# Kernel optimization log

Hardware: AMD Instinct MI355X
Metric: run time of the kernel (lower is better)

Reference implementation:

```python
import jax, jax.numpy as jnp
import numpy as np

N, E, IN, ED, H, L, OUT = 50000, 600000, 16, 4, 128, 4, 3


def setup_inputs() -> dict:
    key = jax.random.key(0)
    ks = jax.random.split(key, 16)
    s = 0.05  # small init scale for numerical stability
    return {
        "x": jax.random.normal(ks[0], (N, IN), jnp.float32),
        "edge_index": jax.random.randint(ks[1], (2, E), 0, N, jnp.int64 if jax.config.jax_enable_x64 else jnp.int32),
        "edge_attr": jax.random.normal(ks[2], (E, ED), jnp.float32),
        "lin_in_w": jax.random.normal(ks[3], (IN, H), jnp.float32) * s,
        "lin_in_b": jnp.zeros((H,), jnp.float32),
        "msg_w1": jax.random.normal(ks[4], (L, H + ED, H), jnp.float32) * s,
        "msg_b1": jnp.zeros((L, H), jnp.float32),
        "msg_w2": jax.random.normal(ks[5], (L, H, H), jnp.float32) * s,
        "msg_b2": jnp.zeros((L, H), jnp.float32),
        "upd_w1": jax.random.normal(ks[6], (L, 2 * H, H), jnp.float32) * s,
        "upd_b1": jnp.zeros((L, H), jnp.float32),
        "upd_w2": jax.random.normal(ks[7], (L, H, H), jnp.float32) * s,
        "upd_b2": jnp.zeros((L, H), jnp.float32),
        "head_w1": jax.random.normal(ks[8], (H, H), jnp.float32) * s,
        "head_b1": jnp.zeros((H,), jnp.float32),
        "head_w2": jax.random.normal(ks[9], (H, OUT), jnp.float32) * s,
        "head_b2": jnp.zeros((OUT,), jnp.float32),
    }


def reference(x, edge_index, edge_attr, lin_in_w, lin_in_b,
              msg_w1, msg_b1, msg_w2, msg_b2,
              upd_w1, upd_b1, upd_w2, upd_b2,
              head_w1, head_b1, head_w2, head_b2):
    n = x.shape[0]
    src, dst = edge_index[0], edge_index[1]  # PyG: message from src (x_j), aggregate at dst
    h = jax.nn.relu(x @ lin_in_w + lin_in_b)  # [N, H]
    # mean-aggregation denominator (0-degree nodes -> divide by 1, sum is 0 anyway)
    cnt = jax.ops.segment_sum(jnp.ones((src.shape[0],), h.dtype), dst, num_segments=n)
    cnt = jnp.maximum(cnt, 1.0)[:, None]
    for l in range(msg_w1.shape[0]):
        mi = jnp.concatenate([h[src], edge_attr], axis=1)          # [E, H+ED] edge gather
        m = jax.nn.relu(mi @ msg_w1[l] + msg_b1[l])
        m = jax.nn.relu(m @ msg_w2[l] + msg_b2[l])                 # [E, H] per-edge message
        agg = jax.ops.segment_sum(m, dst, num_segments=n) / cnt    # [N, H] scatter-mean
        u = jnp.concatenate([h, agg], axis=1)
        u = jax.nn.relu(u @ upd_w1[l] + upd_b1[l])
        u = u @ upd_w2[l] + upd_b2[l]
        h = jax.nn.relu(u + h)  # residual + relu; dropout is eval-mode identity
    o = jax.nn.relu(h @ head_w1 + head_b1)
    return jax.nn.relu(o @ head_w2 + head_b2)  # [N, OUT]
```

## Files before the change

### kernel.cpp

```cpp
#include <hip/hip_runtime.h>


typedef _Float16 f16x8 __attribute__((ext_vector_type(8)));
typedef _Float16 f16x2 __attribute__((ext_vector_type(2)));
typedef __fp16  fp16x2 __attribute__((ext_vector_type(2)));
typedef float f32x4 __attribute__((ext_vector_type(4)));

__device__ inline uint pk2(float a, float b) {
  fp16x2 h = __builtin_amdgcn_cvt_pkrtz(a, b);
  return __builtin_bit_cast(uint, h);
}
__device__ inline ushort f2h(float f) {
  fp16x2 h = __builtin_amdgcn_cvt_pkrtz(f, 0.f);
  return (ushort)__builtin_bit_cast(uint, h);
}
__device__ inline f16x2 bch(uint u) { return __builtin_bit_cast(f16x2, u); }

template <int NT>
__device__ inline void stage_w(ushort* Ws, const ushort* __restrict__ Wt, int t) {
#pragma unroll
  for (int i = t; i < 2048; i += NT) {
    int r = i >> 4, c = i & 15;
    *(uint4*)&Ws[r * 136 + c * 8] = *(const uint4*)&Wt[r * 128 + c * 8];
  }
}
__device__ inline void mfma_4ks(f32x4* acc, const ushort* A, const ushort* Ws,
                                int wave, int lane) {
  int cl = lane & 15, kq = (lane >> 4) * 8;
  int arow = (wave * 16 + cl) * 136;
#pragma unroll
  for (int ks = 0; ks < 4; ++ks) {
    f16x8 af = *(const f16x8*)&A[arow + ks * 32 + kq];
#pragma unroll
    for (int ct = 0; ct < 8; ++ct) {
      f16x8 bf = *(const f16x8*)&Ws[(ct * 16 + cl) * 136 + ks * 32 + kq];
      acc[ct] = __builtin_amdgcn_mfma_f32_16x16x32_f16(af, bf, acc[ct], 0, 0, 0);
    }
  }
}
__device__ inline void mfma_regA(f32x4* acc, const f16x8* af, const ushort* Ws,
                                 int lane) {
  int cl = lane & 15, kq = (lane >> 4) * 8;
#pragma unroll
  for (int ks = 0; ks < 4; ++ks) {
#pragma unroll
    for (int ct = 0; ct < 8; ++ct) {
      f16x8 bf = *(const f16x8*)&Ws[(ct * 16 + cl) * 136 + ks * 32 + kq];
      acc[ct] = __builtin_amdgcn_mfma_f32_16x16x32_f16(af[ks], bf, acc[ct], 0, 0, 0);
    }
  }
}

__global__ __launch_bounds__(256) void count_int_kernel(const int* __restrict__ dst,
                                                        int* __restrict__ cnti, int E) {
  int e = blockIdx.x * 256 + threadIdx.x;
  if (e < E) atomicAdd(&cnti[dst[e]], 1);
}

__global__ __launch_bounds__(256) void scan_block_sum(const int* __restrict__ cnti,
                                                      int* __restrict__ bsum, int N) {
  int i = blockIdx.x * 256 + threadIdx.x;
  int v = (i < N) ? cnti[i] : 0;
#pragma unroll
  for (int o = 1; o < 64; o <<= 1) v += __shfl_xor(v, o);
  __shared__ int wsum[4];
  if ((threadIdx.x & 63) == 0) wsum[threadIdx.x >> 6] = v;
  __syncthreads();
  if (threadIdx.x == 0) bsum[blockIdx.x] = wsum[0] + wsum[1] + wsum[2] + wsum[3];
}
__global__ __launch_bounds__(256) void scan_partials(int* __restrict__ bsum, int nb) {
  __shared__ int s[256];
  int t = threadIdx.x;
  int v = (t < nb) ? bsum[t] : 0;
  s[t] = v;
  __syncthreads();
  for (int o = 1; o < 256; o <<= 1) {
    int u = (t >= o) ? s[t - o] : 0;
    __syncthreads();
    s[t] += u;
    __syncthreads();
  }
  if (t < nb) bsum[t] = s[t] - v;
}
__global__ __launch_bounds__(256) void scan_final(const int* __restrict__ cnti,
                                                  const int* __restrict__ bsum,
                                                  int* __restrict__ rowptr,
                                                  float* __restrict__ invf, int N) {
  __shared__ int s[256];
  int i = blockIdx.x * 256 + threadIdx.x;
  int t = threadIdx.x;
  int v = (i < N) ? cnti[i] : 0;
  s[t] = v;
  __syncthreads();
  for (int o = 1; o < 256; o <<= 1) {
    int u = (t >= o) ? s[t - o] : 0;
    __syncthreads();
    s[t] += u;
    __syncthreads();
  }
  if (i < N) {
    rowptr[i] = bsum[blockIdx.x] + s[t] - v;
    invf[i] = 1.f / (float)max(v, 1);
  }
}

__global__ __launch_bounds__(256) void scatter_kernel(
    const int* __restrict__ src, const int* __restrict__ dst,
    const float4* __restrict__ ea, const int* __restrict__ rowptr,
    int* __restrict__ tmpc, int* __restrict__ srcs, int* __restrict__ dsts,
    float4* __restrict__ eas, int E) {
  int e = blockIdx.x * 256 + threadIdx.x;
  if (e >= E) return;
  int d = dst[e];
  int r = atomicAdd(&tmpc[d], 1);
  int p = rowptr[d] + r;
  srcs[p] = src[e];
  dsts[p] = d;
  eas[p] = ea[e];
}

struct WPtrs { const float* src[22]; };
__global__ __launch_bounds__(256) void wconv_kernel(WPtrs p, ushort* __restrict__ wtb,
                                                    ushort* __restrict__ wlin) {
  int m = blockIdx.y;
  int idx = blockIdx.x * 256 + threadIdx.x;
  if (m == 21) {
    if (idx >= 4096) return;
    int n = idx >> 5, k = idx & 31;
    wlin[idx] = (k < 16) ? f2h(p.src[21][k * 128 + n]) : (ushort)0;
  } else {
    int n = idx >> 7, k = idx & 127;
    wtb[(size_t)m * 16384 + idx] = f2h(p.src[m][k * 128 + n]);
  }
}

__global__ __launch_bounds__(256) void lin_hw_kernel(
    const float* __restrict__ x, const ushort* __restrict__ wlin,
    const float* __restrict__ lb, const ushort* __restrict__ mw1t,
    const float* __restrict__ mb1, float* __restrict__ h,
    ushort* __restrict__ hwb, int N) {
  __shared__ char smem[69632] __attribute__((aligned(16)));
  ushort* xb  = (ushort*)smem;
  ushort* wsl = (ushort*)(smem + 4096);
  ushort* As1 = (ushort*)(smem + 12288);
  ushort* Ws  = (ushort*)(smem + 34816);
  int t = threadIdx.x, lane = t & 63, wave = t >> 6;
  int m0 = blockIdx.x * 64;
  int cl = lane & 15, kq = (lane >> 4) * 8;

  for (int i = t; i < 2048; i += 256) {
    int row = i >> 5, c = i & 31;
    int m = m0 + row;
    xb[i] = (c < 16 && m < N) ? f2h(x[(size_t)m * 16 + c]) : (ushort)0;
  }
  for (int i = t; i < 4096 / 8; i += 256)
    *(uint4*)&wsl[i * 8] = *(const uint4*)&wlin[i * 8];
  stage_w<256>(Ws, mw1t, t);
  __syncthreads();

  f32x4 acc[8];
#pragma unroll
  for (int i = 0; i < 8; ++i)
#pragma unroll
    for (int j = 0; j < 4; ++j) acc[i][j] = 0.f;
  {
    f16x8 af = *(const f16x8*)&xb[(wave * 16 + cl) * 32 + kq];
#pragma unroll
    for (int ct = 0; ct < 8; ++ct) {
      f16x8 bf = *(const f16x8*)&wsl[(ct * 16 + cl) * 32 + kq];
      acc[ct] = __builtin_amdgcn_mfma_f32_16x16x32_f16(af, bf, acc[ct], 0, 0, 0);
    }
  }
#pragma unroll
  for (int reg = 0; reg < 4; ++reg) {
    int row = wave * 16 + (lane >> 4) * 4 + reg;
    int m = m0 + row;
#pragma unroll
    for (int ct = 0; ct < 8; ++ct) {
      int col = ct * 16 + cl;
      float v = fmaxf(acc[ct][reg] + lb[col], 0.f);
      if (m < N) h[(size_t)m * 128 + col] = v;
      As1[row * 136 + col] = f2h(v);
    }
  }
  __syncthreads();
  f32x4 acc2[8];
#pragma unroll
  for (int i = 0; i < 8; ++i)
#pragma unroll
    for (int j = 0; j < 4; ++j) acc2[i][j] = 0.f;
  mfma_4ks(acc2, As1, Ws, wave, lane);
#pragma unroll
  for (int reg = 0; reg < 4; ++reg) {
    int m = m0 + wave * 16 + (lane >> 4) * 4 + reg;
    if (m >= N) continue;
#pragma unroll
    for (int ct = 0; ct < 8; ++ct) {
      int col = ct * 16 + cl;
      hwb[(size_t)m * 128 + col] = f2h(acc2[ct][reg] + mb1[col]);
    }
  }
}

__global__ __launch_bounds__(256, 4) void edge_kernel_v9(
    const ushort* __restrict__ hw, const float4* __restrict__ eas,
    const int* __restrict__ srcs, const int* __restrict__ dsts,
    const ushort* __restrict__ W2t, const float* __restrict__ Wea,
    const float* __restrict__ b2, float* __restrict__ agg, int E) {
  __shared__ ushort Ws[128 * 136];
  __shared__ uint weaH[64][4];
  __shared__ float b2s[128];
  __shared__ int dss[130];
  int t = threadIdx.x, lane = t & 63, wave = t >> 6;
  int cl = lane & 15, g = lane >> 4;
  int p0 = blockIdx.x * 128;
  int base = wave * 32;

  int e0 = p0 + base + cl, e1 = e0 + 16;
  bool v0 = e0 < E, v1 = e1 < E;
  int s0 = v0 ? srcs[e0] : 0, s1 = v1 ? srcs[e1] : 0;
  float4 ea0 = v0 ? eas[e0] : make_float4(0.f, 0.f, 0.f, 0.f);
  float4 ea1 = v1 ? eas[e1] : make_float4(0.f, 0.f, 0.f, 0.f);
  uint4 hv0[4], hv1[4];
  {
    const ushort* h0 = hw + (size_t)s0 * 128 + g * 8;
    const ushort* h1 = hw + (size_t)s1 * 128 + g * 8;
#pragma unroll
    for (int ks = 0; ks < 4; ++ks) {
      hv0[ks] = v0 ? *(const uint4*)&h0[ks * 32] : make_uint4(0, 0, 0, 0);
      hv1[ks] = v1 ? *(const uint4*)&h1[ks * 32] : make_uint4(0, 0, 0, 0);
    }
  }

  stage_w<256>(Ws, W2t, t);
  if (t < 64) {
    weaH[t][0] = pk2(Wea[2 * t], Wea[2 * t + 1]);
    weaH[t][1] = pk2(Wea[128 + 2 * t], Wea[128 + 2 * t + 1]);
    weaH[t][2] = pk2(Wea[256 + 2 * t], Wea[256 + 2 * t + 1]);
    weaH[t][3] = pk2(Wea[384 + 2 * t], Wea[384 + 2 * t + 1]);
  }
  if (t < 128) {
    b2s[t] = b2[t];
    dss[1 + t] = (p0 + t < E) ? dsts[p0 + t] : -1;
  }
  if (t == 0) dss[0] = (p0 > 0) ? dsts[p0 - 1] : -2;
  if (t == 1) dss[129] = (p0 + 128 < E) ? dsts[p0 + 128] : -3;
  __syncthreads();

  uint e0b[4] = {pk2(ea0.x, ea0.x), pk2(ea0.y, ea0.y), pk2(ea0.z, ea0.z), pk2(ea0.w, ea0.w)};
  uint e1b[4] = {pk2(ea1.x, ea1.x), pk2(ea1.y, ea1.y), pk2(ea1.z, ea1.z), pk2(ea1.w, ea1.w)};

  f16x8 af0[4], af1[4];
  f16x2 z2 = {};
#pragma unroll
  for (int ks = 0; ks < 4; ++ks) {
    union { uint u32[4]; f16x8 v; } o0, o1;
    const uint* q0 = (const uint*)&hv0[ks];
    const uint* q1 = (const uint*)&hv1[ks];
    int k2b = ks * 16 + g * 4;
#pragma unroll
    for (int p = 0; p < 4; ++p) {
      uint4 w4 = *(const uint4*)&weaH[k2b + p][0];
      f16x2 m0h = bch(q0[p]);
      f16x2 m1h = bch(q1[p]);
      m0h += bch(e0b[0]) * bch(w4.x); m1h += bch(e1b[0]) * bch(w4.x);
      m0h += bch(e0b[1]) * bch(w4.y); m1h += bch(e1b[1]) * bch(w4.y);
      m0h += bch(e0b[2]) * bch(w4.z); m1h += bch(e1b[2]) * bch(w4.z);
      m0h += bch(e0b[3]) * bch(w4.w); m1h += bch(e1b[3]) * bch(w4.w);
      o0.u32[p] = __builtin_bit_cast(uint, __builtin_elementwise_max(m0h, z2));
      o1.u32[p] = __builtin_bit_cast(uint, __builtin_elementwise_max(m1h, z2));
    }
    af0[ks] = o0.v; af1[ks] = o1.v;
  }

  f32x4 acc0[8], acc1[8];
#pragma unroll
  for (int i = 0; i < 8; ++i)
#pragma unroll
    for (int j = 0; j < 4; ++j) { acc0[i][j] = 0.f; acc1[i][j] = 0.f; }
#pragma unroll
  for (int ks = 0; ks < 4; ++ks) {
#pragma unroll
    for (int ct = 0; ct < 8; ++ct) {
      f16x8 bf = *(const f16x8*)&Ws[(ct * 16 + cl) * 136 + ks * 32 + g * 8];
      acc0[ct] = __builtin_amdgcn_mfma_f32_16x16x32_f16(af0[ks], bf, acc0[ct], 0, 0, 0);
      acc1[ct] = __builtin_amdgcn_mfma_f32_16x16x32_f16(af1[ks], bf, acc1[ct], 0, 0, 0);
    }
  }

#pragma unroll
  for (int ct = 0; ct < 8; ++ct) {
    float bb = b2s[ct * 16 + cl];
#pragma unroll
    for (int reg = 0; reg < 4; ++reg) {
      acc0[ct][reg] = fmaxf(acc0[ct][reg] + bb, 0.f);
      acc1[ct][reg] = fmaxf(acc1[ct][reg] + bb, 0.f);
    }
  }

  int rloc = lane & 31;
  int dmy = dss[1 + base + rloc];
  int dpv = dss[base + rloc];
  int dafter = dss[1 + base + 32];
  unsigned long long bm = __ballot(dmy != dpv);
  unsigned mask32 = (unsigned)bm | 1u;
  bool firstClosed = ((unsigned)bm & 1u) != 0;
  while (mask32) {
    int rOff = __ffs(mask32) - 1;
    unsigned rest = mask32 & (mask32 - 1);
    int eOff = rest ? (__ffs(rest) - 1) : 32;
    mask32 = rest;
    int d = __shfl(dmy, rOff);
    if (d < 0) continue;
    bool openL = (rOff == 0) && !firstClosed;
    bool openR = (eOff == 32) && (dafter == d);
    float ps[8];
#pragma unroll
    for (int ct = 0; ct < 8; ++ct) ps[ct] = 0.f;
#pragma unroll
    for (int reg = 0; reg < 4; ++reg) {
      int r0w = g * 4 + reg;
      bool in0 = (r0w >= rOff) && (r0w < eOff);
      bool in1 = (r0w + 16 >= rOff) && (r0w + 16 < eOff);
#pragma unroll
      for (int ct = 0; ct < 8; ++ct) {
        if (in0) ps[ct] += acc0[ct][reg];
        if (in1) ps[ct] += acc1[ct][reg];
      }
    }
#pragma unroll
    for (int ct = 0; ct < 8; ++ct) {
      ps[ct] += __shfl_xor(ps[ct], 16);
      ps[ct] += __shfl_xor(ps[ct], 32);
    }
    if (g == 0) {
      float* ag = &agg[(size_t)d * 128 + cl];
      if (openL || openR) {
#pragma unroll
        for (int ct = 0; ct < 8; ++ct) atomicAdd(&ag[ct * 16], ps[ct]);
      } else {
#pragma unroll
        for (int ct = 0; ct < 8; ++ct) ag[ct * 16] = ps[ct];
      }
    }
  }
}

__global__ __launch_bounds__(512, 2) void fused_update(
    const float* __restrict__ h, const float* __restrict__ agg,
    const float* __restrict__ inv, const ushort* __restrict__ Wu1a,
    const ushort* __restrict__ Wu1b, const ushort* __restrict__ Wu2,
    const float* __restrict__ b1, const float* __restrict__ b2,
    const ushort* __restrict__ Wn, const float* __restrict__ bn,
    float* __restrict__ h_out, ushort* __restrict__ hwb,
    const float* __restrict__ hw2, const float* __restrict__ hb2,
    float* __restrict__ out, int N, int is_last) {
  __shared__ char smem[69632] __attribute__((aligned(16)));
  ushort* As1 = (ushort*)smem;
  ushort* Ws  = (ushort*)(smem + 34816);
  float* otile = (float*)smem;
  float* w2s   = (float*)(smem + 66560);
  int t = threadIdx.x, lane = t & 63, wave = t >> 6;
  int m0 = blockIdx.x * 128;
  int cl = lane & 15, g = lane >> 4;

  int m2r = m0 + wave * 16 + cl;
  bool mv = m2r < N;
  float sI = mv ? inv[m2r] : 0.f;
  float4 ga[8];
  {
    const float* gp = agg + (size_t)(mv ? m2r : 0) * 128 + g * 8;
#pragma unroll
    for (int ks = 0; ks < 4; ++ks) {
      ga[ks * 2 + 0] = *(const float4*)&gp[ks * 32];
      ga[ks * 2 + 1] = *(const float4*)&gp[ks * 32 + 4];
    }
  }

  {
    int row = t >> 2, q = t & 3;
    int m = m0 + row;
    union { uint u32[16]; uint4 u4[4]; } a;
    if (m < N) {
      const float* hp = h + (size_t)m * 128 + q * 32;
#pragma unroll
      for (int j = 0; j < 8; ++j) {
        float4 hv = *(const float4*)&hp[j * 4];
        a.u32[j * 2 + 0] = pk2(hv.x, hv.y);
        a.u32[j * 2 + 1] = pk2(hv.z, hv.w);
      }
    } else {
#pragma unroll
      for (int j = 0; j < 16; ++j) a.u32[j] = 0;
    }
#pragma unroll
    for (int j = 0; j < 4; ++j)
      *(uint4*)&As1[row * 136 + q * 32 + j * 8] = a.u4[j];
  }
  stage_w<512>(Ws, Wu1a, t);
  __syncthreads();

  f32x4 acc[8];
#pragma unroll
  for (int i = 0; i < 8; ++i)
#pragma unroll
    for (int j = 0; j < 4; ++j) acc[i][j] = 0.f;
  mfma_4ks(acc, As1, Ws, wave, lane);
  __syncthreads();
  stage_w<512>(Ws, Wu1b, t);
  f16x8 af2[4];
#pragma unroll
  for (int ks = 0; ks < 4; ++ks) {
    union { uint u32[4]; f16x8 v; } o;
    const float* f = (const float*)&ga[ks * 2];
#pragma unroll
    for (int j = 0; j < 4; ++j)
      o.u32[j] = pk2(f[j * 2] * sI, f[j * 2 + 1] * sI);
    af2[ks] = o.v;
  }
  __syncthreads();
  mfma_regA(acc, af2, Ws, lane);
  __syncthreads();

#pragma unroll
  for (int reg = 0; reg < 4; ++reg) {
    int row = wave * 16 + g * 4 + reg;
#pragma unroll
    for (int ct = 0; ct < 8; ++ct) {
      int col = ct * 16 + cl;
      As1[row * 136 + col] = f2h(fmaxf(acc[ct][reg] + b1[col], 0.f));
    }
  }
  stage_w<512>(Ws, Wu2, t);
  __syncthreads();

  f32x4 acc2[8];
#pragma unroll
  for (int i = 0; i < 8; ++i)
#pragma unroll
    for (int j = 0; j < 4; ++j) acc2[i][j] = 0.f;
  mfma_4ks(acc2, As1, Ws, wave, lane);
  __syncthreads();

#pragma unroll
  for (int reg = 0; reg < 4; ++reg) {
    int row = wave * 16 + g * 4 + reg;
    int m = m0 + row;
#pragma unroll
    for (int ct = 0; ct < 8; ++ct) {
      int col = ct * 16 + cl;
      float v = acc2[ct][reg] + b2[col];
      if (m < N) v += h[(size_t)m * 128 + col];
      v = fmaxf(v, 0.f);
      if (!is_last && m < N) h_out[(size_t)m * 128 + col] = v;
      As1[row * 136 + col] = f2h(v);
    }
  }
  stage_w<512>(Ws, Wn, t);
  __syncthreads();

  f32x4 acc3[8];
#pragma unroll
  for (int i = 0; i < 8; ++i)
#pragma unroll
    for (int j = 0; j < 4; ++j) acc3[i][j] = 0.f;
  mfma_4ks(acc3, As1, Ws, wave, lane);

  if (!is_last) {
#pragma unroll
    for (int reg = 0; reg < 4; ++reg) {
      int m = m0 + wave * 16 + g * 4 + reg;
      if (m >= N) continue;
#pragma unroll
      for (int ct = 0; ct < 8; ++ct) {
        int col = ct * 16 + cl;
        hwb[(size_t)m * 128 + col] = f2h(acc3[ct][reg] + bn[col]);
      }
    }
  } else {
    __syncthreads();
#pragma unroll
    for (int reg = 0; reg < 4; ++reg) {
      int row = wave * 16 + g * 4 + reg;
#pragma unroll
      for (int ct = 0; ct < 8; ++ct) {
        int col = ct * 16 + cl;
        otile[row * 130 + col] = fmaxf(acc3[ct][reg] + bn[col], 0.f);
      }
    }
    for (int i = t; i < 384; i += 512) w2s[i] = hw2[i];
    __syncthreads();
    if (t < 384) {
      int row = t / 3, c = t % 3;
      int m = m0 + row;
      if (m < N) {
        float s = hb2[c];
#pragma unroll 16
        for (int k = 0; k < 128; ++k) s += otile[row * 130 + k] * w2s[k * 3 + c];
        out[(size_t)m * 3 + c] = fmaxf(s, 0.f);
      }
    }
  }
}

extern "C" void kernel_launch(void* const* d_in, const int* in_sizes, int n_in,
                              void* d_out, int out_size, void* d_ws, size_t ws_size,
                              hipStream_t stream) {
  const float* x       = (const float*)d_in[0];
  const int*   ei      = (const int*)  d_in[1];
  const float* ea      = (const float*)d_in[2];
  const float* lin_w   = (const float*)d_in[3];
  const float* lin_b   = (const float*)d_in[4];
  const float* msg_w1  = (const float*)d_in[5];
  const float* msg_b1  = (const float*)d_in[6];
  const float* msg_w2  = (const float*)d_in[7];
  const float* msg_b2  = (const float*)d_in[8];
  const float* upd_w1  = (const float*)d_in[9];
  const float* upd_b1  = (const float*)d_in[10];
  const float* upd_w2  = (const float*)d_in[11];
  const float* upd_b2  = (const float*)d_in[12];
  const float* head_w1 = (const float*)d_in[13];
  const float* head_b1 = (const float*)d_in[14];
  const float* head_w2 = (const float*)d_in[15];
  const float* head_b2 = (const float*)d_in[16];

  int N = in_sizes[0] / 16;
  int E = in_sizes[1] / 2;
  const int* src = ei;
  const int* dst = ei + E;

  float* ws = (float*)d_ws;
  size_t NH = (size_t)N * 128;
  size_t Nr = ((size_t)N + 4) & ~(size_t)3;
  size_t Er = ((size_t)E + 3) & ~(size_t)3;
  size_t off = 0;
  float*  h    = ws + off; off += NH;
  float*  agg  = ws + off; off += NH;
  float4* eas  = (float4*)(ws + off); off += 4 * Er;
  float*  invf = ws + off; off += Nr;
  ushort* wtb  = (ushort*)(ws + off); off += (size_t)21 * 16384 / 2;
  ushort* wlin = (ushort*)(ws + off); off += 4096 / 2;
  ushort* hwb  = (ushort*)(ws + off); off += NH / 2;
  int*    cnti = (int*)(ws + off); off += Nr;
  int*    tmpc = (int*)(ws + off); off += Nr;
  int*    rowp = (int*)(ws + off); off += Nr;
  int*    srcs = (int*)(ws + off); off += Er;
  int*    dsts = (int*)(ws + off); off += Er;
  int*    bsum = (int*)(ws + off); off += 256;
  float*  out  = (float*)d_out;

  WPtrs wp;
  for (int l = 0; l < 4; ++l) {
    wp.src[l * 5 + 0] = msg_w1 + (size_t)l * 132 * 128;
    wp.src[l * 5 + 1] = msg_w2 + (size_t)l * 128 * 128;
    wp.src[l * 5 + 2] = upd_w1 + (size_t)l * 256 * 128;
    wp.src[l * 5 + 3] = upd_w1 + (size_t)l * 256 * 128 + 128 * 128;
    wp.src[l * 5 + 4] = upd_w2 + (size_t)l * 128 * 128;
  }
  wp.src[20] = head_w1;
  wp.src[21] = lin_w;

  int ngrid = (N + 63) / 64;
  int fgrid = (N + 127) / 128;
  int egrid = (E + 127) / 128;
  int nscan = (N + 255) / 256;

  hipMemsetAsync(cnti, 0, Nr * 4, stream);
  hipMemsetAsync(tmpc, 0, Nr * 4, stream);
  wconv_kernel<<<dim3(64, 22), 256, 0, stream>>>(wp, wtb, wlin);
  count_int_kernel<<<(E + 255) / 256, 256, 0, stream>>>(dst, cnti, E);
  scan_block_sum<<<nscan, 256, 0, stream>>>(cnti, bsum, N);
  scan_partials<<<1, 256, 0, stream>>>(bsum, nscan);
  scan_final<<<nscan, 256, 0, stream>>>(cnti, bsum, rowp, invf, N);
  scatter_kernel<<<(E + 255) / 256, 256, 0, stream>>>(src, dst, (const float4*)ea,
                                                      rowp, tmpc, srcs, dsts, eas, E);
  lin_hw_kernel<<<ngrid, 256, 0, stream>>>(x, wlin, lin_b, wtb, msg_b1, h, hwb, N);

  for (int l = 0; l < 4; ++l) {
    const ushort* mw2t  = wtb + (size_t)(l * 5 + 1) * 16384;
    const ushort* wu1at = wtb + (size_t)(l * 5 + 2) * 16384;
    const ushort* wu1bt = wtb + (size_t)(l * 5 + 3) * 16384;
    const ushort* wu2t  = wtb + (size_t)(l * 5 + 4) * 16384;
    const float*  wea   = msg_w1 + (size_t)l * 132 * 128 + 128 * 128;
    int last = (l == 3);
    const ushort* Wn = last ? (wtb + (size_t)20 * 16384)
                            : (wtb + (size_t)((l + 1) * 5 + 0) * 16384);
    const float* bn = last ? head_b1 : (msg_b1 + (l + 1) * 128);

    hipMemsetAsync(agg, 0, NH * sizeof(float), stream);
    edge_kernel_v9<<<egrid, 256, 0, stream>>>(hwb, eas, srcs, dsts, mw2t, wea,
                                              msg_b2 + l * 128, agg, E);
    fused_update<<<fgrid, 512, 0, stream>>>(h, agg, invf, wu1at, wu1bt, wu2t,
                                            upd_b1 + l * 128, upd_b2 + l * 128,
                                            Wn, bn, h, last ? nullptr : hwb,
                                            head_w2, head_b2, out, N, last);
  }
}
```

Measured before the change: 598.4 us.

## Make edge kernel persistent to amortize weight staging across tiles

The edge message kernel becomes a grid-stride persistent kernel capped at 1024 blocks. Each block stages the 128x128 message weights and edge-attribute weights into LDS once and reuses them across many 128-edge tiles. The destination indices and biases are now read straight from global memory into registers instead of through shared arrays, which removes the per-tile barrier. The trade-off is that the gather loads are no longer overlapped with weight staging, and the fixed grid may balance load less evenly across CUs.

```diff
diff --git a/kernel.cpp b/kernel.cpp
--- a/kernel.cpp
+++ b/kernel.cpp
@@ -202,35 +202,17 @@
   }
 }
 
-__global__ __launch_bounds__(256, 4) void edge_kernel_v9(
+__global__ __launch_bounds__(256, 4) void edge_kernel_v10(
     const ushort* __restrict__ hw, const float4* __restrict__ eas,
     const int* __restrict__ srcs, const int* __restrict__ dsts,
     const ushort* __restrict__ W2t, const float* __restrict__ Wea,
-    const float* __restrict__ b2, float* __restrict__ agg, int E) {
+    const float* __restrict__ b2, float* __restrict__ agg, int E, int ntiles) {
   __shared__ ushort Ws[128 * 136];
   __shared__ uint weaH[64][4];
-  __shared__ float b2s[128];
-  __shared__ int dss[130];
   int t = threadIdx.x, lane = t & 63, wave = t >> 6;
   int cl = lane & 15, g = lane >> 4;
-  int p0 = blockIdx.x * 128;
   int base = wave * 32;
-
-  int e0 = p0 + base + cl, e1 = e0 + 16;
-  bool v0 = e0 < E, v1 = e1 < E;
-  int s0 = v0 ? srcs[e0] : 0, s1 = v1 ? srcs[e1] : 0;
-  float4 ea0 = v0 ? eas[e0] : make_float4(0.f, 0.f, 0.f, 0.f);
-  float4 ea1 = v1 ? eas[e1] : make_float4(0.f, 0.f, 0.f, 0.f);
-  uint4 hv0[4], hv1[4];
-  {
-    const ushort* h0 = hw + (size_t)s0 * 128 + g * 8;
-    const ushort* h1 = hw + (size_t)s1 * 128 + g * 8;
-#pragma unroll
-    for (int ks = 0; ks < 4; ++ks) {
-      hv0[ks] = v0 ? *(const uint4*)&h0[ks * 32] : make_uint4(0, 0, 0, 0);
-      hv1[ks] = v1 ? *(const uint4*)&h1[ks * 32] : make_uint4(0, 0, 0, 0);
-    }
-  }
+  int rloc = lane & 31;
 
   stage_w<256>(Ws, W2t, t);
   if (t < 64) {
@@ -239,108 +221,125 @@
     weaH[t][2] = pk2(Wea[256 + 2 * t], Wea[256 + 2 * t + 1]);
     weaH[t][3] = pk2(Wea[384 + 2 * t], Wea[384 + 2 * t + 1]);
   }
-  if (t < 128) {
-    b2s[t] = b2[t];
-    dss[1 + t] = (p0 + t < E) ? dsts[p0 + t] : -1;
-  }
-  if (t == 0) dss[0] = (p0 > 0) ? dsts[p0 - 1] : -2;
-  if (t == 1) dss[129] = (p0 + 128 < E) ? dsts[p0 + 128] : -3;
-  __syncthreads();
-
-  uint e0b[4] = {pk2(ea0.x, ea0.x), pk2(ea0.y, ea0.y), pk2(ea0.z, ea0.z), pk2(ea0.w, ea0.w)};
-  uint e1b[4] = {pk2(ea1.x, ea1.x), pk2(ea1.y, ea1.y), pk2(ea1.z, ea1.z), pk2(ea1.w, ea1.w)};
-
-  f16x8 af0[4], af1[4];
-  f16x2 z2 = {};
-#pragma unroll
-  for (int ks = 0; ks < 4; ++ks) {
-    union { uint u32[4]; f16x8 v; } o0, o1;
-    const uint* q0 = (const uint*)&hv0[ks];
-    const uint* q1 = (const uint*)&hv1[ks];
-    int k2b = ks * 16 + g * 4;
-#pragma unroll
-    for (int p = 0; p < 4; ++p) {
-      uint4 w4 = *(const uint4*)&weaH[k2b + p][0];
-      f16x2 m0h = bch(q0[p]);
-      f16x2 m1h = bch(q1[p]);
-      m0h += bch(e0b[0]) * bch(w4.x); m1h += bch(e1b[0]) * bch(w4.x);
-      m0h += bch(e0b[1]) * bch(w4.y); m1h += bch(e1b[1]) * bch(w4.y);
-      m0h += bch(e0b[2]) * bch(w4.z); m1h += bch(e1b[2]) * bch(w4.z);
-      m0h += bch(e0b[3]) * bch(w4.w); m1h += bch(e1b[3]) * bch(w4.w);
-      o0.u32[p] = __builtin_bit_cast(uint, __builtin_elementwise_max(m0h, z2));
-      o1.u32[p] = __builtin_bit_cast(uint, __builtin_elementwise_max(m1h, z2));
-    }
-    af0[ks] = o0.v; af1[ks] = o1.v;
-  }
-
-  f32x4 acc0[8], acc1[8];
-#pragma unroll
-  for (int i = 0; i < 8; ++i)
-#pragma unroll
-    for (int j = 0; j < 4; ++j) { acc0[i][j] = 0.f; acc1[i][j] = 0.f; }
-#pragma unroll
-  for (int ks = 0; ks < 4; ++ks) {
-#pragma unroll
-    for (int ct = 0; ct < 8; ++ct) {
-      f16x8 bf = *(const f16x8*)&Ws[(ct * 16 + cl) * 136 + ks * 32 + g * 8];
-      acc0[ct] = __builtin_amdgcn_mfma_f32_16x16x32_f16(af0[ks], bf, acc0[ct], 0, 0, 0);
-      acc1[ct] = __builtin_amdgcn_mfma_f32_16x16x32_f16(af1[ks], bf, acc1[ct], 0, 0, 0);
-    }
-  }
-
-#pragma unroll
-  for (int ct = 0; ct < 8; ++ct) {
-    float bb = b2s[ct * 16 + cl];
-#pragma unroll
-    for (int reg = 0; reg < 4; ++reg) {
-      acc0[ct][reg] = fmaxf(acc0[ct][reg] + bb, 0.f);
-      acc1[ct][reg] = fmaxf(acc1[ct][reg] + bb, 0.f);
-    }
-  }
-
-  int rloc = lane & 31;
-  int dmy = dss[1 + base + rloc];
-  int dpv = dss[base + rloc];
-  int dafter = dss[1 + base + 32];
-  unsigned long long bm = __ballot(dmy != dpv);
-  unsigned mask32 = (unsigned)bm | 1u;
-  bool firstClosed = ((unsigned)bm & 1u) != 0;
-  while (mask32) {
-    int rOff = __ffs(mask32) - 1;
-    unsigned rest = mask32 & (mask32 - 1);
-    int eOff = rest ? (__ffs(rest) - 1) : 32;
-    mask32 = rest;
-    int d = __shfl(dmy, rOff);
-    if (d < 0) continue;
-    bool openL = (rOff == 0) && !firstClosed;
-    bool openR = (eOff == 32) && (dafter == d);
-    float ps[8];
-#pragma unroll
-    for (int ct = 0; ct < 8; ++ct) ps[ct] = 0.f;
-#pragma unroll
-    for (int reg = 0; reg < 4; ++reg) {
-      int r0w = g * 4 + reg;
-      bool in0 = (r0w >= rOff) && (r0w < eOff);
-      bool in1 = (r0w + 16 >= rOff) && (r0w + 16 < eOff);
+  __syncthreads();
+
+  float bb[8];
+#pragma unroll
+  for (int ct = 0; ct < 8; ++ct) bb[ct] = b2[ct * 16 + cl];
+
+  for (int tile = blockIdx.x; tile < ntiles; tile += gridDim.x) {
+    int p0 = tile * 128;
+    int e0 = p0 + base + cl, e1 = e0 + 16;
+    bool v0 = e0 < E, v1 = e1 < E;
+    int s0 = v0 ? srcs[e0] : 0, s1 = v1 ? srcs[e1] : 0;
+    float4 ea0 = v0 ? eas[e0] : make_float4(0.f, 0.f, 0.f, 0.f);
+    float4 ea1 = v1 ? eas[e1] : make_float4(0.f, 0.f, 0.f, 0.f);
+    int idx = p0 + base + rloc;
+    int dmy = (idx < E) ? dsts[idx] : -1;
+    int dpv = (idx == 0) ? -2 : ((idx - 1 < E) ? dsts[idx - 1] : -1);
+    int ia = p0 + base + 32;
+    int dafter = (ia < E) ? dsts[ia] : -3;
+    uint4 hv0[4], hv1[4];
+    {
+      const ushort* h0 = hw + (size_t)s0 * 128 + g * 8;
+      const ushort* h1 = hw + (size_t)s1 * 128 + g * 8;
+#pragma unroll
+      for (int ks = 0; ks < 4; ++ks) {
+        hv0[ks] = v0 ? *(const uint4*)&h0[ks * 32] : make_uint4(0, 0, 0, 0);
+        hv1[ks] = v1 ? *(const uint4*)&h1[ks * 32] : make_uint4(0, 0, 0, 0);
+      }
+    }
+
+    uint e0b[4] = {pk2(ea0.x, ea0.x), pk2(ea0.y, ea0.y), pk2(ea0.z, ea0.z), pk2(ea0.w, ea0.w)};
+    uint e1b[4] = {pk2(ea1.x, ea1.x), pk2(ea1.y, ea1.y), pk2(ea1.z, ea1.z), pk2(ea1.w, ea1.w)};
+
+    f16x8 af0[4], af1[4];
+    f16x2 z2 = {};
+#pragma unroll
+    for (int ks = 0; ks < 4; ++ks) {
+      union { uint u32[4]; f16x8 v; } o0, o1;
+      const uint* q0 = (const uint*)&hv0[ks];
+      const uint* q1 = (const uint*)&hv1[ks];
+      int k2b = ks * 16 + g * 4;
+#pragma unroll
+      for (int p = 0; p < 4; ++p) {
+        uint4 w4 = *(const uint4*)&weaH[k2b + p][0];
+        f16x2 m0h = bch(q0[p]);
+        f16x2 m1h = bch(q1[p]);
+        m0h += bch(e0b[0]) * bch(w4.x); m1h += bch(e1b[0]) * bch(w4.x);
+        m0h += bch(e0b[1]) * bch(w4.y); m1h += bch(e1b[1]) * bch(w4.y);
+        m0h += bch(e0b[2]) * bch(w4.z); m1h += bch(e1b[2]) * bch(w4.z);
+        m0h += bch(e0b[3]) * bch(w4.w); m1h += bch(e1b[3]) * bch(w4.w);
+        o0.u32[p] = __builtin_bit_cast(uint, __builtin_elementwise_max(m0h, z2));
+        o1.u32[p] = __builtin_bit_cast(uint, __builtin_elementwise_max(m1h, z2));
+      }
+      af0[ks] = o0.v; af1[ks] = o1.v;
+    }
+
+    f32x4 acc0[8], acc1[8];
+#pragma unroll
+    for (int i = 0; i < 8; ++i)
+#pragma unroll
+      for (int j = 0; j < 4; ++j) { acc0[i][j] = 0.f; acc1[i][j] = 0.f; }
+#pragma unroll
+    for (int ks = 0; ks < 4; ++ks) {
 #pragma unroll
       for (int ct = 0; ct < 8; ++ct) {
-        if (in0) ps[ct] += acc0[ct][reg];
-        if (in1) ps[ct] += acc1[ct][reg];
-      }
-    }
-#pragma unroll
-    for (int ct = 0; ct < 8; ++ct) {
-      ps[ct] += __shfl_xor(ps[ct], 16);
-      ps[ct] += __shfl_xor(ps[ct], 32);
-    }
-    if (g == 0) {
-      float* ag = &agg[(size_t)d * 128 + cl];
-      if (openL || openR) {
-#pragma unroll
-        for (int ct = 0; ct < 8; ++ct) atomicAdd(&ag[ct * 16], ps[ct]);
-      } else {
-#pragma unroll
-        for (int ct = 0; ct < 8; ++ct) ag[ct * 16] = ps[ct];
+        f16x8 bf = *(const f16x8*)&Ws[(ct * 16 + cl) * 136 + ks * 32 + g * 8];
+        acc0[ct] = __builtin_amdgcn_mfma_f32_16x16x32_f16(af0[ks], bf, acc0[ct], 0, 0, 0);
+        acc1[ct] = __builtin_amdgcn_mfma_f32_16x16x32_f16(af1[ks], bf, acc1[ct], 0, 0, 0);
+      }
+    }
+
+#pragma unroll
+    for (int ct = 0; ct < 8; ++ct) {
+#pragma unroll
+      for (int reg = 0; reg < 4; ++reg) {
+        acc0[ct][reg] = fmaxf(acc0[ct][reg] + bb[ct], 0.f);
+        acc1[ct][reg] = fmaxf(acc1[ct][reg] + bb[ct], 0.f);
+      }
+    }
+
+    unsigned long long bmv = __ballot(dmy != dpv);
+    unsigned mask32 = (unsigned)bmv | 1u;
+    bool firstClosed = ((unsigned)bmv & 1u) != 0;
+    while (mask32) {
+      int rOff = __ffs(mask32) - 1;
+      unsigned rest = mask32 & (mask32 - 1);
+      int eOff = rest ? (__ffs(rest) - 1) : 32;
+      mask32 = rest;
+      int d = __shfl(dmy, rOff);
+      if (d < 0) continue;
+      bool openL = (rOff == 0) && !firstClosed;
+      bool openR = (eOff == 32) && (dafter == d);
+      float ps[8];
+#pragma unroll
+      for (int ct = 0; ct < 8; ++ct) ps[ct] = 0.f;
+#pragma unroll
+      for (int reg = 0; reg < 4; ++reg) {
+        int r0w = g * 4 + reg;
+        bool in0 = (r0w >= rOff) && (r0w < eOff);
+        bool in1 = (r0w + 16 >= rOff) && (r0w + 16 < eOff);
+#pragma unroll
+        for (int ct = 0; ct < 8; ++ct) {
+          if (in0) ps[ct] += acc0[ct][reg];
+          if (in1) ps[ct] += acc1[ct][reg];
+        }
+      }
+#pragma unroll
+      for (int ct = 0; ct < 8; ++ct) {
+        ps[ct] += __shfl_xor(ps[ct], 16);
+        ps[ct] += __shfl_xor(ps[ct], 32);
+      }
+      if (g == 0) {
+        float* ag = &agg[(size_t)d * 128 + cl];
+        if (openL || openR) {
+#pragma unroll
+          for (int ct = 0; ct < 8; ++ct) atomicAdd(&ag[ct * 16], ps[ct]);
+        } else {
+#pragma unroll
+          for (int ct = 0; ct < 8; ++ct) ag[ct * 16] = ps[ct];
+        }
       }
     }
   }
@@ -562,7 +561,8 @@
 
   int ngrid = (N + 63) / 64;
   int fgrid = (N + 127) / 128;
-  int egrid = (E + 127) / 128;
+  int ntiles = (E + 127) / 128;
+  int egrid = ntiles < 1024 ? ntiles : 1024;
   int nscan = (N + 255) / 256;
 
   hipMemsetAsync(cnti, 0, Nr * 4, stream);
@@ -588,8 +588,8 @@
     const float* bn = last ? head_b1 : (msg_b1 + (l + 1) * 128);
 
     hipMemsetAsync(agg, 0, NH * sizeof(float), stream);
-    edge_kernel_v9<<<egrid, 256, 0, stream>>>(hwb, eas, srcs, dsts, mw2t, wea,
-                                              msg_b2 + l * 128, agg, E);
+    edge_kernel_v10<<<egrid, 256, 0, stream>>>(hwb, eas, srcs, dsts, mw2t, wea,
+                                               msg_b2 + l * 128, agg, E, ntiles);
     fused_update<<<fgrid, 512, 0, stream>>>(h, agg, invf, wu1at, wu1bt, wu2t,
                                             upd_b1 + l * 128, upd_b2 + l * 128,
                                             Wn, bn, h, last ? nullptr : hwb,
```

Measured after the change: 1.444 ms. 141% more time.
